# Kernel optimization log

Measured on AMD Instinct MI355X. Metric: run time of the kernel, lower is better.

The kernel has to match this reference:

```python
import jax, jax.numpy as jnp
import numpy as np

DIM = 256
NUM_HEADS = 8
SCALE = (DIM // NUM_HEADS) ** -0.5  # matches torch: head_dim**-0.5, even though no head split happens
THRESH = 0.6


def setup_inputs() -> dict:
    key = jax.random.key(0)
    ks = jax.random.split(key, 6)
    B, N = 4, 4096
    x = jax.random.normal(ks[0], (B, N, DIM), dtype=jnp.float32)
    y = jax.random.normal(ks[1], (B, N, DIM), dtype=jnp.float32)
    s = DIM ** -0.5
    Wq = jax.random.normal(ks[2], (DIM, DIM), dtype=jnp.float32) * s
    Wk = jax.random.normal(ks[3], (DIM, DIM), dtype=jnp.float32) * s
    Wv = jax.random.normal(ks[4], (DIM, DIM), dtype=jnp.float32) * s
    Wp = jax.random.normal(ks[5], (DIM, DIM), dtype=jnp.float32) * s
    bp = jnp.zeros((DIM,), dtype=jnp.float32)
    return {"x": x, "y": y, "Wq": Wq, "Wk": Wk, "Wv": Wv, "Wp": Wp, "bp": bp}


def reference(x, y, Wq, Wk, Wv, Wp, bp):
    # q,v from x; k from y (cross attention, no head split — faithful to source)
    q = jnp.einsum('bnd,de->bne', x, Wq)
    k = jnp.einsum('bnd,de->bne', y, Wk)
    v = jnp.einsum('bnd,de->bne', x, Wv)
    attn = jnp.einsum('bnd,bmd->bnm', q, k) * SCALE  # [B, N, N]
    attn = jax.nn.softmax(attn, axis=-1)
    attn = jnp.where(attn < THRESH, jnp.zeros((), attn.dtype), attn)  # hard threshold
    out = jnp.einsum('bnm,bmd->bnd', attn, v)
    out = jnp.einsum('bnd,de->bne', out, Wp) + bp
    return out
```

## Files before the change

kernel.cpp:

```cpp
#include <hip/hip_runtime.h>
#include <cstdint>
#include <cmath>

#define DIM     256
#define NSEQ    4096
#define SCALE   0.17677669529663687f
#define THRESH  0.6f
#define BAND    0.01f
#define MAXSUSP 8000

using half8 = __attribute__((ext_vector_type(8))) _Float16;
using half4 = __attribute__((ext_vector_type(4))) _Float16;
using f32x4 = __attribute__((ext_vector_type(4))) float;

__global__ void prep_kernel(const float* __restrict__ W0, const float* __restrict__ W1,
                            const float* __restrict__ W2, const float* __restrict__ W3,
                            float* __restrict__ Wt, _Float16* __restrict__ Wth,
                            int* __restrict__ susp)
{
    __shared__ float tile[64][68];
    int t = threadIdx.x;
    int m = blockIdx.x >> 4;
    int ti = blockIdx.x & 15;
    int tr = (ti >> 2) * 64, tc = (ti & 3) * 64;
    const float* W = (m == 0) ? W0 : (m == 1) ? W1 : (m == 2) ? W2 : W3;
    if (blockIdx.x == 0 && t < 2) susp[t] = 0;
    int rr = t >> 4, c4 = (t & 15) * 4;
#pragma unroll
    for (int p = 0; p < 4; ++p) {
        int row = p * 16 + rr;
        *(float4*)&tile[row][c4] = *(const float4*)(W + (size_t)(tr + row) * DIM + tc + c4);
    }
    __syncthreads();
#pragma unroll
    for (int p = 0; p < 4; ++p) {
        int c = p * 16 + rr;
        float4 v;
        v.x = tile[c4 + 0][c]; v.y = tile[c4 + 1][c];
        v.z = tile[c4 + 2][c]; v.w = tile[c4 + 3][c];
        size_t ot = (size_t)(tc + c) * DIM + tr + c4;
        if (m == 0) *(float4*)(Wt + ot) = v;
        half4 hv;
        hv[0] = (_Float16)v.x; hv[1] = (_Float16)v.y;
        hv[2] = (_Float16)v.z; hv[3] = (_Float16)v.w;
        *(half4*)(Wth + (size_t)m * 65536 + ot) = hv;
    }
}

__global__ __launch_bounds__(256, 2)
void proj3_mfma(const float* __restrict__ x, const float* __restrict__ y,
                const _Float16* __restrict__ Wth,
                _Float16* __restrict__ qh, _Float16* __restrict__ kh,
                float* __restrict__ kf, _Float16* __restrict__ vh)
{
    __shared__ half8 sA[1024];
    __shared__ half8 sB[1024];
    int tid = threadIdx.x, w = tid >> 6, ln = tid & 63;
    int rb = blockIdx.x * 128, cb = blockIdx.y * 128, m = blockIdx.z;
    const float* A = (m == 1) ? y : x;
    const _Float16* B = Wth + (size_t)m * 65536;

    f32x4 acc[2][8];
#pragma unroll
    for (int mi = 0; mi < 2; ++mi)
#pragma unroll
        for (int nt = 0; nt < 8; ++nt) acc[mi][nt] = (f32x4){0.f, 0.f, 0.f, 0.f};

    int r = tid >> 1;
    int chalf = (tid & 1) * 4;
    for (int kc = 0; kc < 4; ++kc) {
        __syncthreads();
        const float*    asrc = A + (size_t)(rb + r) * DIM + kc * 64 + chalf * 8;
        const _Float16* bsrc = B + (size_t)(cb + r) * DIM + kc * 64 + chalf * 8;
#pragma unroll
        for (int cc = 0; cc < 4; ++cc) {
            int c = chalf + cc;
            float4 f0 = *(const float4*)(asrc + cc * 8);
            float4 f1 = *(const float4*)(asrc + cc * 8 + 4);
            half8 hv;
            hv[0] = (_Float16)f0.x; hv[1] = (_Float16)f0.y; hv[2] = (_Float16)f0.z; hv[3] = (_Float16)f0.w;
            hv[4] = (_Float16)f1.x; hv[5] = (_Float16)f1.y; hv[6] = (_Float16)f1.z; hv[7] = (_Float16)f1.w;
            int li = ((r >> 4) * 2 + (c >> 2)) * 64 + ((c & 3) << 4) + (r & 15);
            sA[li] = hv;
            sB[li] = *(const half8*)(bsrc + cc * 8);
        }
        __syncthreads();
#pragma unroll
        for (int s = 0; s < 2; ++s) {
            half8 a0 = sA[((w * 2 + 0) * 2 + s) * 64 + ln];
            half8 a1 = sA[((w * 2 + 1) * 2 + s) * 64 + ln];
#pragma unroll
            for (int nt = 0; nt < 8; ++nt) {
                half8 bv = sB[(nt * 2 + s) * 64 + ln];
                acc[0][nt] = __builtin_amdgcn_mfma_f32_16x16x32_f16(a0, bv, acc[0][nt], 0, 0, 0);
                acc[1][nt] = __builtin_amdgcn_mfma_f32_16x16x32_f16(a1, bv, acc[1][nt], 0, 0, 0);
            }
        }
    }
    int quad = ln >> 4, cix = ln & 15;
#pragma unroll
    for (int mi = 0; mi < 2; ++mi)
#pragma unroll
        for (int nt = 0; nt < 8; ++nt)
#pragma unroll
            for (int rr = 0; rr < 4; ++rr) {
                int row = rb + (w * 2 + mi) * 16 + quad * 4 + rr;
                int col = cb + nt * 16 + cix;
                size_t off = (size_t)row * DIM + col;
                float vv = acc[mi][nt][rr];
                if (m == 0)      qh[off] = (_Float16)vv;
                else if (m == 1) { kh[off] = (_Float16)vv; kf[off] = vv; }
                else             vh[off] = (_Float16)vv;
            }
}

__global__ __launch_bounds__(256, 2)
void flash_fp16(const _Float16* __restrict__ qh, const _Float16* __restrict__ kh,
                float* __restrict__ pm, float* __restrict__ pl, int* __restrict__ pam)
{
    __shared__ half8 sK[4096];
    int tid = threadIdx.x, w = tid >> 6, ln = tid & 63;
    int g = blockIdx.x;
    int qt = blockIdx.y;
    int ms = g & 3, b = g >> 2;
    size_t qbase = (size_t)b * NSEQ + qt * 128 + w * 32;
    size_t krow0 = (size_t)b * NSEQ + ms * 1024;

    half8 qf[2][8];
#pragma unroll
    for (int mi = 0; mi < 2; ++mi) {
        const _Float16* qsrc = qh + (qbase + mi * 16 + (ln & 15)) * DIM + (ln >> 4) * 8;
#pragma unroll
        for (int ks = 0; ks < 8; ++ks)
            qf[mi][ks] = *(const half8*)(qsrc + ks * 32);
    }

    float rm[2][4], rl[2][4]; int ram[2][4];
#pragma unroll
    for (int mi = 0; mi < 2; ++mi)
#pragma unroll
        for (int rr = 0; rr < 4; ++rr) { rm[mi][rr] = -INFINITY; rl[mi][rr] = 0.f; ram[mi][rr] = 0; }

    int r = tid >> 1, h = tid & 1;
    int nt_ = r >> 4, m_ = r & 15;
    for (int kt = 0; kt < 8; ++kt) {
        __syncthreads();
        const _Float16* ksrc = kh + (krow0 + kt * 128 + r) * DIM + h * 128;
#pragma unroll
        for (int cc = 0; cc < 16; ++cc) {
            int c = h * 16 + cc;
            sK[(nt_ * 8 + (c >> 2)) * 64 + ((c & 3) << 4) + m_] = *(const half8*)(ksrc + cc * 8);
        }
        __syncthreads();

        f32x4 acc[2][8];
#pragma unroll
        for (int mi = 0; mi < 2; ++mi)
#pragma unroll
            for (int nt = 0; nt < 8; ++nt) acc[mi][nt] = (f32x4){0.f, 0.f, 0.f, 0.f};

#pragma unroll
        for (int nt = 0; nt < 8; ++nt)
#pragma unroll
            for (int ks = 0; ks < 8; ++ks) {
                half8 bk = sK[(nt * 8 + ks) * 64 + ln];
                acc[0][nt] = __builtin_amdgcn_mfma_f32_16x16x32_f16(qf[0][ks], bk, acc[0][nt], 0, 0, 0);
                acc[1][nt] = __builtin_amdgcn_mfma_f32_16x16x32_f16(qf[1][ks], bk, acc[1][nt], 0, 0, 0);
            }

        int keybase = b * NSEQ + ms * 1024 + kt * 128 + (ln & 15);
#pragma unroll
        for (int mi = 0; mi < 2; ++mi)
#pragma unroll
            for (int rr = 0; rr < 4; ++rr) {
                float mx = rm[mi][rr]; int amx = ram[mi][rr];
                float sv[8];
#pragma unroll
                for (int nt = 0; nt < 8; ++nt) {
                    sv[nt] = acc[mi][nt][rr] * SCALE;
                    if (sv[nt] > mx) { mx = sv[nt]; amx = keybase + nt * 16; }
                }
                float sum = 0.f;
#pragma unroll
                for (int nt = 0; nt < 8; ++nt) sum += __expf(sv[nt] - mx);
                rl[mi][rr] = rl[mi][rr] * __expf(rm[mi][rr] - mx) + sum;
                rm[mi][rr] = mx; ram[mi][rr] = amx;
            }
    }

#pragma unroll
    for (int mi = 0; mi < 2; ++mi)
#pragma unroll
        for (int rr = 0; rr < 4; ++rr) {
            float m0 = rm[mi][rr], l0 = rl[mi][rr]; int am0 = ram[mi][rr];
#pragma unroll
            for (int d = 1; d < 16; d <<= 1) {
                float m2 = __shfl_xor(m0, d);
                float l2 = __shfl_xor(l0, d);
                int  am2 = __shfl_xor(am0, d);
                if (m2 > m0) { l0 = l0 * __expf(m0 - m2) + l2; m0 = m2; am0 = am2; }
                else         { l0 = l0 + l2 * __expf(m2 - m0); }
            }
            if ((ln & 15) == 0) {
                int row = b * NSEQ + qt * 128 + w * 32 + mi * 16 + (ln >> 4) * 4 + rr;
                pm[row * 4 + ms] = m0; pl[row * 4 + ms] = l0; pam[row * 4 + ms] = am0;
            }
        }
}

__global__ void merge_kernel(const float* __restrict__ pm, const float* __restrict__ pl,
                             const int* __restrict__ pam,
                             float* __restrict__ scl, int* __restrict__ sidx,
                             int* __restrict__ susp)
{
    int row = blockIdx.x * 256 + threadIdx.x;
    float m = -INFINITY, l = 0.f; int am = 0;
#pragma unroll
    for (int s = 0; s < 4; ++s) {
        float m2 = pm[row * 4 + s];
        float l2 = pl[row * 4 + s];
        int  am2 = pam[row * 4 + s];
        if (m2 > m) { l = l * __expf(m - m2) + l2; m = m2; am = am2; }
        else        { l = l + l2 * __expf(m2 - m); }
    }
    float p = 1.f / l;
    scl[row] = (p >= THRESH) ? p : 0.f;
    sidx[row] = am;
    if (fabsf(p - THRESH) < BAND) {
        int i = atomicAdd(susp, 1);
        if (i < MAXSUSP) susp[2 + i] = row;
    }
}

__global__ __launch_bounds__(256)
void recheck_kernel(const float* __restrict__ x, const float* __restrict__ Wtq,
                    const float* __restrict__ kf, const int* __restrict__ susp,
                    float* __restrict__ scl, int* __restrict__ sidx)
{
    __shared__ float qrow[DIM];
    __shared__ float rmw[4], rlw[4]; __shared__ int raw_[4];
    int tid = threadIdx.x;
    int count = susp[0]; if (count > MAXSUSP) count = MAXSUSP;

    for (int i = blockIdx.x; i < count; i += gridDim.x) {
        int row = susp[2 + i];
        int bb = row >> 12;
        __syncthreads();
        {
            const float* xr = x + (size_t)row * DIM;
            const float* wr = Wtq + (size_t)tid * DIM;
            float a = 0.f;
            for (int d = 0; d < DIM; d += 4) {
                float4 xv = *(const float4*)(xr + d);
                float4 wv = *(const float4*)(wr + d);
                a = fmaf(xv.x, wv.x, a); a = fmaf(xv.y, wv.y, a);
                a = fmaf(xv.z, wv.z, a); a = fmaf(xv.w, wv.w, a);
            }
            qrow[tid] = a;
        }
        __syncthreads();

        int c = tid & 7, g = tid >> 3;
        float m = -INFINITY, l = 0.f; int am = 0;
        for (int n0 = 0; n0 < NSEQ; n0 += 32) {
            int n = n0 + g;
            const float* kr = kf + ((size_t)bb * NSEQ + n) * DIM;
            float dot = 0.f;
#pragma unroll
            for (int j = 0; j < 8; ++j) {
                int d = (j * 8 + c) * 4;
                float4 kv = *(const float4*)(kr + d);
                dot = fmaf(qrow[d], kv.x, dot);     dot = fmaf(qrow[d + 1], kv.y, dot);
                dot = fmaf(qrow[d + 2], kv.z, dot); dot = fmaf(qrow[d + 3], kv.w, dot);
            }
#pragma unroll
            for (int dd = 1; dd < 8; dd <<= 1) dot += __shfl_xor(dot, dd);
            float s = dot * SCALE;
            if (s > m) { l = l * __expf(m - s) + 1.f; m = s; am = bb * NSEQ + n; }
            else       { l += __expf(s - m); }
        }
#pragma unroll
        for (int dd = 8; dd < 64; dd <<= 1) {
            float m2 = __shfl_xor(m, dd); float l2 = __shfl_xor(l, dd); int a2 = __shfl_xor(am, dd);
            if (m2 > m) { l = l * __expf(m - m2) + l2; m = m2; am = a2; }
            else        { l += l2 * __expf(m2 - m); }
        }
        if ((tid & 63) == 0) { rmw[tid >> 6] = m; rlw[tid >> 6] = l; raw_[tid >> 6] = am; }
        __syncthreads();
        if (tid == 0) {
            float M = rmw[0], L = rlw[0]; int A = raw_[0];
            for (int wv = 1; wv < 4; ++wv) {
                float m2 = rmw[wv], l2 = rlw[wv]; int a2 = raw_[wv];
                if (m2 > M) { L = L * __expf(M - m2) + l2; M = m2; A = a2; }
                else        { L += l2 * __expf(m2 - M); }
            }
            float p = 1.f / L;
            scl[row] = (p >= THRESH) ? p : 0.f;
            sidx[row] = A;
        }
    }
}

__global__ __launch_bounds__(256, 2)
void out_mfma(const _Float16* __restrict__ vh, const _Float16* __restrict__ Wph,
              const float* __restrict__ scl, const int* __restrict__ sidx,
              const float* __restrict__ bp, float* __restrict__ out)
{
    __shared__ half8 sA[1024];
    __shared__ half8 sB[1024];
    int tid = threadIdx.x, w = tid >> 6, ln = tid & 63;
    int rb = blockIdx.x * 128, cb = blockIdx.y * 128;

    f32x4 acc[2][8];
#pragma unroll
    for (int mi = 0; mi < 2; ++mi)
#pragma unroll
        for (int nt = 0; nt < 8; ++nt) acc[mi][nt] = (f32x4){0.f, 0.f, 0.f, 0.f};

    int r = tid >> 1, chalf = (tid & 1) * 4;
    int gix = sidx[rb + r];
    for (int kc = 0; kc < 4; ++kc) {
        __syncthreads();
        const _Float16* asrc = vh + (size_t)gix * DIM + kc * 64 + chalf * 8;
        const _Float16* bsrc = Wph + (size_t)(cb + r) * DIM + kc * 64 + chalf * 8;
#pragma unroll
        for (int cc = 0; cc < 4; ++cc) {
            int c = chalf + cc;
            int li = ((r >> 4) * 2 + (c >> 2)) * 64 + ((c & 3) << 4) + (r & 15);
            sA[li] = *(const half8*)(asrc + cc * 8);
            sB[li] = *(const half8*)(bsrc + cc * 8);
        }
        __syncthreads();
#pragma unroll
        for (int s = 0; s < 2; ++s) {
            half8 a0 = sA[((w * 2 + 0) * 2 + s) * 64 + ln];
            half8 a1 = sA[((w * 2 + 1) * 2 + s) * 64 + ln];
#pragma unroll
            for (int nt = 0; nt < 8; ++nt) {
                half8 bv = sB[(nt * 2 + s) * 64 + ln];
                acc[0][nt] = __builtin_amdgcn_mfma_f32_16x16x32_f16(a0, bv, acc[0][nt], 0, 0, 0);
                acc[1][nt] = __builtin_amdgcn_mfma_f32_16x16x32_f16(a1, bv, acc[1][nt], 0, 0, 0);
            }
        }
    }
    int quad = ln >> 4, cix = ln & 15;
#pragma unroll
    for (int mi = 0; mi < 2; ++mi)
#pragma unroll
        for (int rr = 0; rr < 4; ++rr) {
            int row = rb + (w * 2 + mi) * 16 + quad * 4 + rr;
            float sc = scl[row];
#pragma unroll
            for (int nt = 0; nt < 8; ++nt) {
                int col = cb + nt * 16 + cix;
                out[(size_t)row * DIM + col] = acc[mi][nt][rr] * sc + bp[col];
            }
        }
}

extern "C" void kernel_launch(void* const* d_in, const int* in_sizes, int n_in,
                              void* d_out, int out_size, void* d_ws, size_t ws_size,
                              hipStream_t stream)
{
    (void)in_sizes; (void)n_in; (void)out_size; (void)ws_size;
    const float* x  = (const float*)d_in[0];
    const float* y  = (const float*)d_in[1];
    const float* Wq = (const float*)d_in[2];
    const float* Wk = (const float*)d_in[3];
    const float* Wv = (const float*)d_in[4];
    const float* Wp = (const float*)d_in[5];
    const float* bp = (const float*)d_in[6];
    float* out = (float*)d_out;

    float* p0 = (float*)d_ws;
    float* kf = p0;                 p0 += 4194304;
    float* Wt = p0;                 p0 += 65536;
    _Float16* Wth = (_Float16*)p0;  p0 += 4 * 65536 / 2;
    _Float16* qh  = (_Float16*)p0;  p0 += 2097152;
    _Float16* kh  = (_Float16*)p0;  p0 += 2097152;
    _Float16* vh  = (_Float16*)p0;  p0 += 2097152;
    float* pm  = p0;                p0 += 65536;
    float* pl  = p0;                p0 += 65536;
    int*  pam  = (int*)p0;          p0 += 65536;
    float* scl = p0;                p0 += 16384;
    int*  sidx = (int*)p0;          p0 += 16384;
    int*  susp = (int*)p0;

    prep_kernel<<<64, 256, 0, stream>>>(Wq, Wk, Wv, Wp, Wt, Wth, susp);
    proj3_mfma<<<dim3(128, 2, 3), 256, 0, stream>>>(x, y, Wth, qh, kh, kf, vh);
    flash_fp16<<<dim3(16, 32), 256, 0, stream>>>(qh, kh, pm, pl, pam);
    merge_kernel<<<64, 256, 0, stream>>>(pm, pl, pam, scl, sidx, susp);
    recheck_kernel<<<256, 256, 0, stream>>>(x, Wt, kf, susp, scl, sidx);
    out_mfma<<<dim3(128, 2), 256, 0, stream>>>(vh, Wth + 3 * 65536, scl, sidx, bp, out);
}
```

Baseline: 259.3 us.

## Split suspect-row recheck into q-projection, chunked partial softmax, and fold kernels

The recheck of rows whose max probability lies near the threshold is split into three kernels. The first computes fp32 q for each suspect row, the second splits the 4096 keys into 32 chunks across a 2D grid to produce partial max/sum/argmax, and the third merges the chunks. The goal is to spread each row's long sequential key scan over many blocks and so raise parallelism and memory-level concurrency. In exchange it adds two launches and workspace traffic for the intermediate q and partial results.

```diff
diff --git a/kernel.cpp b/kernel.cpp
--- a/kernel.cpp
+++ b/kernel.cpp
@@ -8,6 +8,7 @@
 #define THRESH  0.6f
 #define BAND    0.01f
 #define MAXSUSP 8000
+#define NCHUNK  32
 
 using half8 = __attribute__((ext_vector_type(8))) _Float16;
 using half4 = __attribute__((ext_vector_type(4))) _Float16;
@@ -233,71 +234,105 @@
 }
 
 __global__ __launch_bounds__(256)
-void recheck_kernel(const float* __restrict__ x, const float* __restrict__ Wtq,
-                    const float* __restrict__ kf, const int* __restrict__ susp,
-                    float* __restrict__ scl, int* __restrict__ sidx)
-{
-    __shared__ float qrow[DIM];
-    __shared__ float rmw[4], rlw[4]; __shared__ int raw_[4];
+void recheck_q(const float* __restrict__ x, const float* __restrict__ Wtq,
+               const int* __restrict__ susp, float* __restrict__ qsusp)
+{
     int tid = threadIdx.x;
     int count = susp[0]; if (count > MAXSUSP) count = MAXSUSP;
-
     for (int i = blockIdx.x; i < count; i += gridDim.x) {
         int row = susp[2 + i];
+        const float* xr = x + (size_t)row * DIM;
+        const float* wr = Wtq + (size_t)tid * DIM;
+        float a = 0.f;
+        for (int d = 0; d < DIM; d += 4) {
+            float4 xv = *(const float4*)(xr + d);
+            float4 wv = *(const float4*)(wr + d);
+            a = fmaf(xv.x, wv.x, a); a = fmaf(xv.y, wv.y, a);
+            a = fmaf(xv.z, wv.z, a); a = fmaf(xv.w, wv.w, a);
+        }
+        qsusp[(size_t)i * DIM + tid] = a;
+    }
+}
+
+__global__ __launch_bounds__(256)
+void recheck_part(const float* __restrict__ qsusp, const float* __restrict__ kf,
+                  const int* __restrict__ susp,
+                  float* __restrict__ pmP, float* __restrict__ plP, int* __restrict__ pamP)
+{
+    __shared__ float qs[DIM];
+    __shared__ float wm[4], wl[4]; __shared__ int wa[4];
+    int tid = threadIdx.x;
+    int chunk = blockIdx.x;
+    int count = susp[0]; if (count > MAXSUSP) count = MAXSUSP;
+
+    for (int i = blockIdx.y; i < count; i += gridDim.y) {
+        int row = susp[2 + i];
         int bb = row >> 12;
         __syncthreads();
-        {
-            const float* xr = x + (size_t)row * DIM;
-            const float* wr = Wtq + (size_t)tid * DIM;
-            float a = 0.f;
-            for (int d = 0; d < DIM; d += 4) {
-                float4 xv = *(const float4*)(xr + d);
-                float4 wv = *(const float4*)(wr + d);
-                a = fmaf(xv.x, wv.x, a); a = fmaf(xv.y, wv.y, a);
-                a = fmaf(xv.z, wv.z, a); a = fmaf(xv.w, wv.w, a);
-            }
-            qrow[tid] = a;
-        }
-        __syncthreads();
-
-        int c = tid & 7, g = tid >> 3;
-        float m = -INFINITY, l = 0.f; int am = 0;
-        for (int n0 = 0; n0 < NSEQ; n0 += 32) {
-            int n = n0 + g;
-            const float* kr = kf + ((size_t)bb * NSEQ + n) * DIM;
-            float dot = 0.f;
-#pragma unroll
-            for (int j = 0; j < 8; ++j) {
-                int d = (j * 8 + c) * 4;
-                float4 kv = *(const float4*)(kr + d);
-                dot = fmaf(qrow[d], kv.x, dot);     dot = fmaf(qrow[d + 1], kv.y, dot);
-                dot = fmaf(qrow[d + 2], kv.z, dot); dot = fmaf(qrow[d + 3], kv.w, dot);
-            }
-#pragma unroll
-            for (int dd = 1; dd < 8; dd <<= 1) dot += __shfl_xor(dot, dd);
-            float s = dot * SCALE;
-            if (s > m) { l = l * __expf(m - s) + 1.f; m = s; am = bb * NSEQ + n; }
-            else       { l += __expf(s - m); }
-        }
-#pragma unroll
-        for (int dd = 8; dd < 64; dd <<= 1) {
-            float m2 = __shfl_xor(m, dd); float l2 = __shfl_xor(l, dd); int a2 = __shfl_xor(am, dd);
+        qs[tid] = qsusp[(size_t)i * DIM + tid];
+        __syncthreads();
+
+        int key = tid >> 1, h = tid & 1;
+        int gkey = bb * NSEQ + chunk * 128 + key;
+        const float* kr = kf + (size_t)gkey * DIM + h * 128;
+        const float* qp = qs + h * 128;
+        float dot = 0.f;
+#pragma unroll
+        for (int j = 0; j < 32; ++j) {
+            float4 kv = *(const float4*)(kr + j * 4);
+            float4 qv = *(const float4*)(qp + j * 4);
+            dot = fmaf(qv.x, kv.x, dot); dot = fmaf(qv.y, kv.y, dot);
+            dot = fmaf(qv.z, kv.z, dot); dot = fmaf(qv.w, kv.w, dot);
+        }
+        dot += __shfl_xor(dot, 1);
+        float s = dot * SCALE;
+
+        float m = (h == 0) ? s : -INFINITY;
+        float l = (h == 0) ? 1.f : 0.f;
+        int  am = (h == 0) ? gkey : 0;
+#pragma unroll
+        for (int d = 1; d < 64; d <<= 1) {
+            float m2 = __shfl_xor(m, d);
+            float l2 = __shfl_xor(l, d);
+            int  a2 = __shfl_xor(am, d);
             if (m2 > m) { l = l * __expf(m - m2) + l2; m = m2; am = a2; }
-            else        { l += l2 * __expf(m2 - m); }
-        }
-        if ((tid & 63) == 0) { rmw[tid >> 6] = m; rlw[tid >> 6] = l; raw_[tid >> 6] = am; }
+            else        { l = l + l2 * __expf(m2 - m); }
+        }
+        if ((tid & 63) == 0) { wm[tid >> 6] = m; wl[tid >> 6] = l; wa[tid >> 6] = am; }
         __syncthreads();
         if (tid == 0) {
-            float M = rmw[0], L = rlw[0]; int A = raw_[0];
+            float M = wm[0], L = wl[0]; int A = wa[0];
+#pragma unroll
             for (int wv = 1; wv < 4; ++wv) {
-                float m2 = rmw[wv], l2 = rlw[wv]; int a2 = raw_[wv];
+                float m2 = wm[wv], l2 = wl[wv]; int a2 = wa[wv];
                 if (m2 > M) { L = L * __expf(M - m2) + l2; M = m2; A = a2; }
                 else        { L += l2 * __expf(m2 - M); }
             }
-            float p = 1.f / L;
-            scl[row] = (p >= THRESH) ? p : 0.f;
-            sidx[row] = A;
-        }
+            size_t o = (size_t)i * NCHUNK + chunk;
+            pmP[o] = M; plP[o] = L; pamP[o] = A;
+        }
+    }
+}
+
+__global__ __launch_bounds__(256)
+void recheck_fold(const float* __restrict__ pmP, const float* __restrict__ plP,
+                  const int* __restrict__ pamP, const int* __restrict__ susp,
+                  float* __restrict__ scl, int* __restrict__ sidx)
+{
+    int count = susp[0]; if (count > MAXSUSP) count = MAXSUSP;
+    for (int i = blockIdx.x * 256 + threadIdx.x; i < count; i += gridDim.x * 256) {
+        float M = -INFINITY, L = 0.f; int A = 0;
+#pragma unroll
+        for (int c = 0; c < NCHUNK; ++c) {
+            size_t o = (size_t)i * NCHUNK + c;
+            float m2 = pmP[o], l2 = plP[o]; int a2 = pamP[o];
+            if (m2 > M) { L = L * __expf(M - m2) + l2; M = m2; A = a2; }
+            else        { L += l2 * __expf(m2 - M); }
+        }
+        float p = 1.f / L;
+        int row = susp[2 + i];
+        scl[row] = (p >= THRESH) ? p : 0.f;
+        sidx[row] = A;
     }
 }
 
@@ -384,12 +419,18 @@
     int*  pam  = (int*)p0;          p0 += 65536;
     float* scl = p0;                p0 += 16384;
     int*  sidx = (int*)p0;          p0 += 16384;
-    int*  susp = (int*)p0;
+    int*  susp = (int*)p0;          p0 += MAXSUSP + 2 + 2;
+    float* qsusp = p0;              p0 += (size_t)MAXSUSP * DIM;
+    float* pmP = p0;                p0 += (size_t)MAXSUSP * NCHUNK;
+    float* plP = p0;                p0 += (size_t)MAXSUSP * NCHUNK;
+    int*  pamP = (int*)p0;
 
     prep_kernel<<<64, 256, 0, stream>>>(Wq, Wk, Wv, Wp, Wt, Wth, susp);
     proj3_mfma<<<dim3(128, 2, 3), 256, 0, stream>>>(x, y, Wth, qh, kh, kf, vh);
     flash_fp16<<<dim3(16, 32), 256, 0, stream>>>(qh, kh, pm, pl, pam);
     merge_kernel<<<64, 256, 0, stream>>>(pm, pl, pam, scl, sidx, susp);
-    recheck_kernel<<<256, 256, 0, stream>>>(x, Wt, kf, susp, scl, sidx);
+    recheck_q<<<128, 256, 0, stream>>>(x, Wt, susp, qsusp);
+    recheck_part<<<dim3(NCHUNK, 64), 256, 0, stream>>>(qsusp, kf, susp, pmP, plP, pamP);
+    recheck_fold<<<8, 256, 0, stream>>>(pmP, plP, pamP, susp, scl, sidx);
     out_mfma<<<dim3(128, 2), 256, 0, stream>>>(vh, Wth + 3 * 65536, scl, sidx, bp, out);
 }
```

Result: faster. 226.7 us (-12.6%).
